# Performance work log

Hardware: AMD Instinct MI355X
Metric: run time of the kernel (lower is better)

## Reference

```python
import jax, jax.numpy as jnp
import numpy as np

N_NODES = 50000
N_EDGES = 1600000
D = 64          # n_atom_basis = n_filters
NB = 25         # n_basis (RBF)
L = 3           # n_interactions
CUTOFF = 5.0
MAX_Z = 100


def swish(x):
    return x * jax.nn.sigmoid(x)


def setup_inputs() -> dict:
    key = jax.random.key(0)
    ks = jax.random.split(key, 20)
    z = jax.random.randint(ks[0], (N_NODES,), 0, MAX_Z)
    src = jax.random.randint(ks[1], (N_EDGES,), 0, N_NODES)
    dst = jax.random.randint(ks[2], (N_EDGES,), 0, N_NODES)
    rij = jax.random.uniform(ks[3], (N_EDGES,), jnp.float32, 0.3, CUTOFF)
    s = 1.0 / np.sqrt(D)
    emb = jax.random.normal(ks[4], (MAX_Z, D), jnp.float32) * 0.1
    emb = emb.at[0].set(0.0)  # padding_idx=0
    Win = jax.random.normal(ks[5], (L, D, D), jnp.float32) * s
    Wf1 = jax.random.normal(ks[6], (L, NB, D), jnp.float32) * (1.0 / np.sqrt(NB))
    bf1 = jnp.zeros((L, D), jnp.float32)
    Wf2 = jax.random.normal(ks[7], (L, D, D), jnp.float32) * s
    bf2 = jnp.zeros((L, D), jnp.float32)
    Wo1 = jax.random.normal(ks[8], (L, D, D), jnp.float32) * s
    bo1 = jnp.zeros((L, D), jnp.float32)
    Wo2 = jax.random.normal(ks[9], (L, D, D), jnp.float32) * s
    bo2 = jnp.zeros((L, D), jnp.float32)
    gn_alpha = jnp.ones((L, D), jnp.float32)
    gn_gamma = jnp.ones((L, D), jnp.float32)
    gn_beta = jnp.zeros((L, D), jnp.float32)
    return dict(z=z, src=src, dst=dst, rij=rij, emb=emb, Win=Win,
                Wf1=Wf1, bf1=bf1, Wf2=Wf2, bf2=bf2,
                Wo1=Wo1, bo1=bo1, Wo2=Wo2, bo2=bo2,
                gn_alpha=gn_alpha, gn_gamma=gn_gamma, gn_beta=gn_beta)


def reference(z, src, dst, rij, emb, Win, Wf1, bf1, Wf2, bf2,
              Wo1, bo1, Wo2, bo2, gn_alpha, gn_gamma, gn_beta):
    n = z.shape[0]
    # GaussianSmearing(0, cutoff, n_basis)
    offsets = jnp.linspace(0.0, CUTOFF, NB)
    width = offsets[1] - offsets[0]
    coeff = -0.5 / (width * width)
    fij = jnp.exp(coeff * (rij[:, None] - offsets[None, :]) ** 2)  # [E, NB]
    # CosineCutoff
    C = 0.5 * (jnp.cos(rij * (np.pi / CUTOFF)) + 1.0) * (rij < CUTOFF)  # [E]

    feat = emb[z]  # [N, D]
    for l in range(L):
        # cfconv: in2f (no bias), filter MLP gated by cutoff, gather*W, scatter-sum
        x1 = feat @ Win[l]                                            # [N, D]
        W = swish(fij @ Wf1[l] + bf1[l]) @ Wf2[l] + bf2[l]            # [E, D]
        W = W * C[:, None]
        m = x1[src] * W                                               # [E, D]
        agg = jax.ops.segment_sum(m, dst, num_segments=n)             # [N, D]
        # f2out: Dense+swish, Dense; residual
        y = swish(agg @ Wo1[l] + bo1[l]) @ Wo2[l] + bo2[l]
        feat = feat + y
        # GraphNorm over all nodes (single graph)
        mean = feat.mean(axis=0)
        h = feat - gn_alpha[l] * mean
        var = (h * h).mean(axis=0)
        feat = gn_gamma[l] * h * jax.lax.rsqrt(var + 1e-5) + gn_beta[l]

    # softmax readout: per-feature attention over nodes
    w = jax.nn.softmax(feat, axis=0)
    pooled = (w * feat).sum(axis=0)  # [D]
    return feat, pooled
```

## Files before the change

### kernel.cpp

```cpp
#include <hip/hip_runtime.h>
#include <hip/hip_bf16.h>
#include <math.h>

#define D64 64
#define KTAB 4096
#define TROWS (KTAB + 1)

typedef unsigned int uint4a __attribute__((ext_vector_type(4), aligned(4)));
typedef __attribute__((ext_vector_type(8))) short bf16x8;
typedef __attribute__((ext_vector_type(4))) float f32x4;

__device__ __forceinline__ void atomAddF(float* p, float v) {
  __hip_atomic_fetch_add(p, v, __ATOMIC_RELAXED, __HIP_MEMORY_SCOPE_AGENT);
}
__device__ __forceinline__ float swishf(float x) { return x / (1.0f + expf(-x)); }
__device__ __forceinline__ float bx(unsigned short s) {
  return __uint_as_float((unsigned)s << 16);
}
__device__ __forceinline__ unsigned short f2b(float f) {
  unsigned u = __float_as_uint(f);
  return (unsigned short)((u + 0x7FFFu + ((u >> 16) & 1u)) >> 16);
}

__global__ void k_init(const int* __restrict__ z, const float* __restrict__ emb,
                       float* __restrict__ feat, int total) {
  int idx = blockIdx.x * 256 + threadIdx.x;
  if (idx < total) feat[idx] = emb[z[idx >> 6] * D64 + (idx & 63)];
}

__global__ void k_wprep(const float* __restrict__ Win, const float* __restrict__ Wo1,
                        const float* __restrict__ Wo2, unsigned short* __restrict__ Wb) {
  int idx = blockIdx.x * 256 + threadIdx.x;
  if (idx >= 3 * 3 * 64 * 8) return;
  const int fr = idx & 7;
  const int lane = (idx >> 3) & 63;
  const int m = (idx >> 9) % 3;
  const int l = idx / 1536;
  const int ct = fr >> 1, ks = fr & 1;
  const int c = ct * 16 + (lane & 15);
  const int k0 = ks * 32 + (lane >> 4) * 8;
  const float* W = (m == 0 ? Win : (m == 1 ? Wo1 : Wo2)) + (size_t)l * D64 * D64;
  unsigned short* o = &Wb[(size_t)((l * 3 + m) * 64 + lane) * 64 + fr * 8];
#pragma unroll
  for (int j = 0; j < 8; ++j) o[j] = f2b(W[(k0 + j) * D64 + c]);
}

__global__ __launch_bounds__(256) void k_hist64(const int* __restrict__ dst,
                                                int* __restrict__ bcnt, int E) {
  __shared__ int c[64];
  if (threadIdx.x < 64) c[threadIdx.x] = 0;
  __syncthreads();
  const int step = gridDim.x * blockDim.x * 4;
  for (int i = (blockIdx.x * blockDim.x + threadIdx.x) * 4; i < E; i += step) {
    if (i + 4 <= E) {
      int4 d = *(const int4*)&dst[i];
      atomicAdd(&c[d.x >> 10], 1);
      atomicAdd(&c[d.y >> 10], 1);
      atomicAdd(&c[d.z >> 10], 1);
      atomicAdd(&c[d.w >> 10], 1);
    } else {
      for (int q = i; q < E; ++q) atomicAdd(&c[dst[q] >> 10], 1);
    }
  }
  __syncthreads();
  if (threadIdx.x < 64 && c[threadIdx.x] > 0)
    atomicAdd(&bcnt[threadIdx.x], c[threadIdx.x]);
}

__global__ void k_scan64(const int* __restrict__ bcnt, int* __restrict__ bbase,
                         int* __restrict__ gcur) {
  const int t = threadIdx.x;
  int v = bcnt[t];
  int x = v;
  for (int o = 1; o < 64; o <<= 1) {
    int y = __shfl_up(x, o);
    if (t >= o) x += y;
  }
  bbase[t] = x - v;
  gcur[t] = x - v;
  if (t == 63) bbase[64] = x;
}

__global__ __launch_bounds__(256) void k_part(const int* __restrict__ src,
                                              const int* __restrict__ dst,
                                              const float* __restrict__ rij,
                                              int* __restrict__ gcur,
                                              uint2* __restrict__ rec, int E) {
  __shared__ uint2 ord[2048];
  __shared__ unsigned char obk[2048];
  __shared__ int cnt[64], cbase[64], cpos[64], gpos[64];
  __shared__ int tot_s;
  const int tid = threadIdx.x;
  for (int c = blockIdx.x; c * 2048 < E; c += gridDim.x) {
    const int s0 = c * 2048;
    if (tid < 64) cnt[tid] = 0;
    __syncthreads();
    const int i0 = s0 + tid * 8;
    int dd[8], ss[8];
    float rr[8];
    bool val[8];
    if (i0 + 8 <= E) {
      int4 d0 = *(const int4*)&dst[i0];
      int4 d1 = *(const int4*)&dst[i0 + 4];
      int4 sa = *(const int4*)&src[i0];
      int4 sb2 = *(const int4*)&src[i0 + 4];
      float4 r0 = *(const float4*)&rij[i0];
      float4 r1 = *(const float4*)&rij[i0 + 4];
      dd[0] = d0.x; dd[1] = d0.y; dd[2] = d0.z; dd[3] = d0.w;
      dd[4] = d1.x; dd[5] = d1.y; dd[6] = d1.z; dd[7] = d1.w;
      ss[0] = sa.x; ss[1] = sa.y; ss[2] = sa.z; ss[3] = sa.w;
      ss[4] = sb2.x; ss[5] = sb2.y; ss[6] = sb2.z; ss[7] = sb2.w;
      rr[0] = r0.x; rr[1] = r0.y; rr[2] = r0.z; rr[3] = r0.w;
      rr[4] = r1.x; rr[5] = r1.y; rr[6] = r1.z; rr[7] = r1.w;
#pragma unroll
      for (int q = 0; q < 8; ++q) val[q] = true;
    } else {
#pragma unroll
      for (int q = 0; q < 8; ++q) {
        int i = i0 + q;
        val[q] = (i < E);
        if (val[q]) { dd[q] = dst[i]; ss[q] = src[i]; rr[q] = rij[i]; }
        else { dd[q] = 0; ss[q] = 0; rr[q] = 0.0f; }
      }
    }
    int bk[8];
    unsigned ry[8];
#pragma unroll
    for (int q = 0; q < 8; ++q) {
      bk[q] = dd[q] >> 10;
      int k = (int)(rr[q] * ((float)KTAB * 0.2f) + 0.5f);
      if (k > KTAB) k = KTAB;
      ry[q] = ((unsigned)ss[q] << 16) | (unsigned)k;
      if (val[q]) atomicAdd(&cnt[bk[q]], 1);
    }
    __syncthreads();
    if (tid < 64) {
      int v = cnt[tid];
      int x = v;
      for (int o = 1; o < 64; o <<= 1) {
        int y = __shfl_up(x, o);
        if (tid >= o) x += y;
      }
      cbase[tid] = x - v;
      cpos[tid] = x - v;
      if (tid == 63) tot_s = x;
    }
    __syncthreads();
#pragma unroll
    for (int q = 0; q < 8; ++q) {
      if (val[q]) {
        int slot = atomicAdd(&cpos[bk[q]], 1);
        ord[slot] = make_uint2((unsigned)dd[q], ry[q]);
        obk[slot] = (unsigned char)bk[q];
      }
    }
    __syncthreads();
    if (tid < 64 && cnt[tid] > 0) gpos[tid] = atomicAdd(&gcur[tid], cnt[tid]);
    __syncthreads();
    const int tot = tot_s;
    for (int t = tid; t < tot; t += 256) {
      int b2 = obk[t];
      rec[gpos[b2] + (t - cbase[b2])] = ord[t];
    }
    __syncthreads();
  }
}

__global__ __launch_bounds__(1024) void k_build(const uint2* __restrict__ rec,
                                                const int* __restrict__ bbase,
                                                int* __restrict__ rp,
                                                unsigned* __restrict__ ep, int n) {
  __shared__ int cnt[1024];
  __shared__ int curl[1024];
  const int tid = threadIdx.x;
  const int b = blockIdx.x;
  const int lo = bbase[b], hi = bbase[b + 1];
  cnt[tid] = 0;
  __syncthreads();
  for (int i = lo + tid; i < hi; i += 1024)
    atomicAdd(&cnt[rec[i].x & 1023], 1);
  __syncthreads();
  const int v = cnt[tid];
  for (int o = 1; o < 1024; o <<= 1) {
    int t = (tid >= o) ? cnt[tid - o] : 0;
    __syncthreads();
    cnt[tid] += t;
    __syncthreads();
  }
  const int excl = cnt[tid] - v;
  curl[tid] = excl;
  const int node = (b << 10) + tid;
  if (node <= n) rp[node] = lo + excl;
  __syncthreads();
  for (int i = lo + tid; i < hi; i += 1024) {
    uint2 e = rec[i];
    int pos = lo + atomicAdd(&curl[e.x & 1023], 1);
    ep[pos] = e.y;
  }
}

__global__ __launch_bounds__(256) void k_tables(const float* __restrict__ Wf1,
                                                const float* __restrict__ bf1,
                                                const float* __restrict__ Wf2,
                                                const float* __restrict__ bf2,
                                                __hip_bfloat16* __restrict__ Tb) {
  __shared__ float w1[25 * D64];
  __shared__ float w2[D64 * D64];
  __shared__ float rb[4][D64];
  const int lane = threadIdx.x & 63;
  const int wsl = threadIdx.x >> 6;
  const int l = blockIdx.x / 129;
  const int gb = blockIdx.x % 129;
  for (int i = threadIdx.x; i < 25 * D64; i += 256) w1[i] = Wf1[l * 25 * D64 + i];
  for (int i = threadIdx.x; i < D64 * D64; i += 256) w2[i] = Wf2[l * D64 * D64 + i];
  __syncthreads();
  const float bias1 = bf1[l * D64 + lane];
  const float bias2 = bf2[l * D64 + lane];
  const float width = 5.0f / 24.0f;
  const float coeff = -0.5f / (width * width);
  for (int gi = 0; gi < 8; ++gi) {
    const int g = gb * 32 + wsl * 8 + gi;
    if (g >= TROWS) break;
    const float r = (float)g * (5.0f / KTAB);
    float fv = 0.0f;
    if (lane < 25) { float ddv = r - (float)lane * width; fv = expf(coeff * ddv * ddv); }
    rb[wsl][lane] = fv;
    float a1 = bias1;
#pragma unroll
    for (int b = 0; b < 25; ++b)
      a1 = fmaf(rb[wsl][b], w1[b * D64 + lane], a1);
    float sw = swishf(a1);
    rb[wsl][lane] = sw;
    float a2 = bias2;
#pragma unroll
    for (int k = 0; k < D64; ++k)
      a2 = fmaf(rb[wsl][k], w2[k * D64 + lane], a2);
    float C = (r < 5.0f) ? 0.5f * (cosf(r * 0.62831853f) + 1.0f) : 0.0f;
    Tb[(size_t)(l * TROWS + g) * D64 + lane] = __float2bfloat16(a2 * C);
  }
}

__global__ void k_nid(float* __restrict__ stats) {
  int d = threadIdx.x;
  stats[128 + d] = 1.0f;
  stats[192 + d] = 0.0f;
}

__global__ __launch_bounds__(256) void k_x1(const float* __restrict__ feat,
                                            const unsigned short* __restrict__ Wb,
                                            const float* __restrict__ stats,
                                            __hip_bfloat16* __restrict__ x1, int n) {
  const int lane = threadIdx.x & 63;
  const int r16 = lane & 15;
  const int kg = lane >> 4;
  unsigned short* __restrict__ x1u = (unsigned short*)x1;
  const unsigned short* wl = Wb + (size_t)lane * 64;
  bf16x8 bw[4][2];
#pragma unroll
  for (int ct = 0; ct < 4; ++ct)
#pragma unroll
    for (int ks = 0; ks < 2; ++ks)
      bw[ct][ks] = *(const bf16x8*)&wl[(ct * 2 + ks) * 8];
  float sca[2][8], sha[2][8];
#pragma unroll
  for (int ks = 0; ks < 2; ++ks) {
    const int k0 = ks * 32 + kg * 8;
#pragma unroll
    for (int j = 0; j < 8; ++j) {
      sca[ks][j] = stats[128 + k0 + j];
      sha[ks][j] = stats[192 + k0 + j];
    }
  }
  const int ntile = (n + 15) >> 4;
  const int wid = (blockIdx.x * blockDim.x + threadIdx.x) >> 6;
  const int nw = (gridDim.x * blockDim.x) >> 6;
  for (int t = wid; t < ntile; t += nw) {
    const int base = t * 16;
    int ra = base + r16; if (ra > n - 1) ra = n - 1;
    bf16x8 a[2];
#pragma unroll
    for (int ks = 0; ks < 2; ++ks) {
      const float* p = &feat[(size_t)ra * D64 + ks * 32 + kg * 8];
      bf16x8 v;
#pragma unroll
      for (int j = 0; j < 8; ++j) v[j] = (short)f2b(fmaf(p[j], sca[ks][j], sha[ks][j]));
      a[ks] = v;
    }
    f32x4 acc[4];
#pragma unroll
    for (int ct = 0; ct < 4; ++ct) {
      f32x4 z = {0.0f, 0.0f, 0.0f, 0.0f};
      z = __builtin_amdgcn_mfma_f32_16x16x32_bf16(a[0], bw[ct][0], z, 0, 0, 0);
      z = __builtin_amdgcn_mfma_f32_16x16x32_bf16(a[1], bw[ct][1], z, 0, 0, 0);
      acc[ct] = z;
    }
#pragma unroll
    for (int ct = 0; ct < 4; ++ct)
#pragma unroll
      for (int r = 0; r < 4; ++r) {
        const int rm = base + kg * 4 + r;
        if (rm < n) x1u[(size_t)rm * D64 + ct * 16 + r16] = f2b(acc[ct][r]);
      }
  }
}

__global__ __launch_bounds__(256) void k_gather(const __hip_bfloat16* __restrict__ x1,
                                                const __hip_bfloat16* __restrict__ Tb,
                                                const unsigned* __restrict__ ep,
                                                const int* __restrict__ rp,
                                                unsigned short* __restrict__ aggb, int n) {
  const int lane = threadIdx.x & 63;
  const int half = lane >> 5;
  const int fl = lane & 31;
  const unsigned short* __restrict__ x1u = (const unsigned short*)x1;
  const unsigned short* __restrict__ Tu = (const unsigned short*)Tb;
  const int wid = (blockIdx.x * blockDim.x + threadIdx.x) >> 6;
  const int nw = (gridDim.x * blockDim.x) >> 6;
  for (int nd = wid; nd < n; nd += nw) {
    const int j0 = rp[nd], j1 = rp[nd + 1];
    float ax0 = 0.0f, ay0 = 0.0f, ax1 = 0.0f, ay1 = 0.0f;
    int j = j0;
    for (; j + 8 <= j1; j += 8) {
      const uint4a uu = *(const uint4a*)(ep + j + 4 * half);
      const unsigned u0 = uu.x, u1 = uu.y, u2 = uu.z, u3 = uu.w;
      const ushort2 xA = *(const ushort2*)&x1u[(size_t)(u0 >> 16) * D64 + fl * 2];
      const ushort2 xB = *(const ushort2*)&x1u[(size_t)(u1 >> 16) * D64 + fl * 2];
      const ushort2 xC = *(const ushort2*)&x1u[(size_t)(u2 >> 16) * D64 + fl * 2];
      const ushort2 xD = *(const ushort2*)&x1u[(size_t)(u3 >> 16) * D64 + fl * 2];
      const ushort2 tA = *(const ushort2*)&Tu[(size_t)(u0 & 0x1FFFu) * D64 + fl * 2];
      const ushort2 tB = *(const ushort2*)&Tu[(size_t)(u1 & 0x1FFFu) * D64 + fl * 2];
      const ushort2 tC = *(const ushort2*)&Tu[(size_t)(u2 & 0x1FFFu) * D64 + fl * 2];
      const ushort2 tD = *(const ushort2*)&Tu[(size_t)(u3 & 0x1FFFu) * D64 + fl * 2];
      ax0 = fmaf(bx(xA.x), bx(tA.x), ax0);
      ay0 = fmaf(bx(xA.y), bx(tA.y), ay0);
      ax1 = fmaf(bx(xB.x), bx(tB.x), ax1);
      ay1 = fmaf(bx(xB.y), bx(tB.y), ay1);
      ax0 = fmaf(bx(xC.x), bx(tC.x), ax0);
      ay0 = fmaf(bx(xC.y), bx(tC.y), ay0);
      ax1 = fmaf(bx(xD.x), bx(tD.x), ax1);
      ay1 = fmaf(bx(xD.y), bx(tD.y), ay1);
    }
    for (; j + 2 <= j1; j += 2) {
      const unsigned u = ep[j + half];
      const ushort2 xr = *(const ushort2*)&x1u[(size_t)(u >> 16) * D64 + fl * 2];
      const ushort2 tw = *(const ushort2*)&Tu[(size_t)(u & 0x1FFFu) * D64 + fl * 2];
      ax0 = fmaf(bx(xr.x), bx(tw.x), ax0);
      ay0 = fmaf(bx(xr.y), bx(tw.y), ay0);
    }
    if (j < j1 && half == 0) {
      const unsigned u = ep[j];
      const ushort2 xr = *(const ushort2*)&x1u[(size_t)(u >> 16) * D64 + fl * 2];
      const ushort2 tw = *(const ushort2*)&Tu[(size_t)(u & 0x1FFFu) * D64 + fl * 2];
      ax0 = fmaf(bx(xr.x), bx(tw.x), ax0);
      ay0 = fmaf(bx(xr.y), bx(tw.y), ay0);
    }
    float ax = ax0 + ax1, ay = ay0 + ay1;
    ax += __shfl_xor(ax, 32);
    ay += __shfl_xor(ay, 32);
    if (half == 0) {
      unsigned pk = ((unsigned)f2b(ay) << 16) | (unsigned)f2b(ax);
      *(unsigned*)&aggb[(size_t)nd * D64 + fl * 2] = pk;
    }
  }
}

__global__ __launch_bounds__(256) void k_out(const unsigned short* __restrict__ aggb,
                                             const unsigned short* __restrict__ Wb1,
                                             const unsigned short* __restrict__ Wb2,
                                             const float* __restrict__ bo1,
                                             const float* __restrict__ bo2,
                                             const float* __restrict__ nstats,
                                             float* __restrict__ feat,
                                             float* __restrict__ part, int n) {
  __shared__ __align__(16) unsigned short tl[4][16 * 72];
  __shared__ float redp[4][128];
  const int lane = threadIdx.x & 63;
  const int wsl = threadIdx.x >> 6;
  const int r16 = lane & 15;
  const int kg = lane >> 4;
  const unsigned short* wl1 = Wb1 + (size_t)lane * 64;
  const unsigned short* wl2 = Wb2 + (size_t)lane * 64;
  bf16x8 bw1[4][2], bw2[4][2];
#pragma unroll
  for (int ct = 0; ct < 4; ++ct)
#pragma unroll
    for (int ks = 0; ks < 2; ++ks) {
      bw1[ct][ks] = *(const bf16x8*)&wl1[(ct * 2 + ks) * 8];
      bw2[ct][ks] = *(const bf16x8*)&wl2[(ct * 2 + ks) * 8];
    }
  float b1c[4], b2c[4], scc[4], shc[4];
#pragma unroll
  for (int ct = 0; ct < 4; ++ct) {
    b1c[ct] = bo1[ct * 16 + r16];
    b2c[ct] = bo2[ct * 16 + r16];
    scc[ct] = nstats[128 + ct * 16 + r16];
    shc[ct] = nstats[192 + ct * 16 + r16];
  }
  float sf[4] = {0, 0, 0, 0}, sf2[4] = {0, 0, 0, 0};
  unsigned short* tw = tl[wsl];
  const int ntile = (n + 15) >> 4;
  const int wid = (blockIdx.x * blockDim.x + threadIdx.x) >> 6;
  const int nw = (gridDim.x * blockDim.x) >> 6;
  for (int t = wid; t < ntile; t += nw) {
    const int base = t * 16;
    int ra = base + r16; if (ra > n - 1) ra = n - 1;
    bf16x8 a1[2];
#pragma unroll
    for (int ks = 0; ks < 2; ++ks)
      a1[ks] = *(const bf16x8*)&aggb[(size_t)ra * D64 + ks * 32 + kg * 8];
    f32x4 acc[4];
#pragma unroll
    for (int ct = 0; ct < 4; ++ct) {
      f32x4 z = {0.0f, 0.0f, 0.0f, 0.0f};
      z = __builtin_amdgcn_mfma_f32_16x16x32_bf16(a1[0], bw1[ct][0], z, 0, 0, 0);
      z = __builtin_amdgcn_mfma_f32_16x16x32_bf16(a1[1], bw1[ct][1], z, 0, 0, 0);
      acc[ct] = z;
    }
#pragma unroll
    for (int ct = 0; ct < 4; ++ct)
#pragma unroll
      for (int r = 0; r < 4; ++r)
        tw[(kg * 4 + r) * 72 + ct * 16 + r16] = f2b(swishf(acc[ct][r] + b1c[ct]));
    bf16x8 a2[2];
#pragma unroll
    for (int ks = 0; ks < 2; ++ks)
      a2[ks] = *(const bf16x8*)&tw[r16 * 72 + ks * 32 + kg * 8];
    f32x4 acc2[4];
#pragma unroll
    for (int ct = 0; ct < 4; ++ct) {
      f32x4 z = {0.0f, 0.0f, 0.0f, 0.0f};
      z = __builtin_amdgcn_mfma_f32_16x16x32_bf16(a2[0], bw2[ct][0], z, 0, 0, 0);
      z = __builtin_amdgcn_mfma_f32_16x16x32_bf16(a2[1], bw2[ct][1], z, 0, 0, 0);
      acc2[ct] = z;
    }
#pragma unroll
    for (int ct = 0; ct < 4; ++ct)
#pragma unroll
      for (int r = 0; r < 4; ++r) {
        const int rm = base + kg * 4 + r;
        if (rm < n) {
          const size_t ix = (size_t)rm * D64 + ct * 16 + r16;
          float fv = fmaf(feat[ix], scc[ct], shc[ct]);
          float fn = fv + acc2[ct][r] + b2c[ct];
          feat[ix] = fn;
          sf[ct] += fn;
          sf2[ct] += fn * fn;
        }
      }
  }
#pragma unroll
  for (int ct = 0; ct < 4; ++ct) {
    sf[ct] += __shfl_xor(sf[ct], 16);
    sf[ct] += __shfl_xor(sf[ct], 32);
    sf2[ct] += __shfl_xor(sf2[ct], 16);
    sf2[ct] += __shfl_xor(sf2[ct], 32);
  }
  if (kg == 0) {
#pragma unroll
    for (int ct = 0; ct < 4; ++ct) {
      redp[wsl][ct * 16 + r16] = sf[ct];
      redp[wsl][64 + ct * 16 + r16] = sf2[ct];
    }
  }
  __syncthreads();
  if (threadIdx.x < 128) {
    float v = redp[0][threadIdx.x] + redp[1][threadIdx.x] +
              redp[2][threadIdx.x] + redp[3][threadIdx.x];
    atomAddF(&part[(blockIdx.x & 63) * 128 + threadIdx.x], v);
  }
}

__global__ void k_nfin(float* __restrict__ part, float* __restrict__ stats,
                       const float* __restrict__ al, const float* __restrict__ ga,
                       const float* __restrict__ be, int n) {
  const int t = threadIdx.x;
  float s = 0.0f;
#pragma unroll 8
  for (int b = 0; b < 64; ++b) s += part[b * 128 + t];
  __shared__ float red[128];
  red[t] = s;
#pragma unroll 8
  for (int b = 0; b < 64; ++b) part[b * 128 + t] = 0.0f;
  __syncthreads();
  if (t < 64) {
    float invN = 1.0f / (float)n;
    float mu = red[t] * invN;
    float ex2 = red[64 + t] * invN;
    float a = al[t];
    float var = ex2 - (2.0f * a - a * a) * mu * mu;
    float sc = ga[t] * rsqrtf(var + 1e-5f);
    stats[128 + t] = sc;
    stats[192 + t] = be[t] - sc * a * mu;
  }
}

__global__ __launch_bounds__(256) void k_pool(float* __restrict__ feat,
                                              const float* __restrict__ stats,
                                              float* __restrict__ part, int n) {
  __shared__ float redp[4][128];
  const int lane = threadIdx.x & 63;
  const int wsl = threadIdx.x >> 6;
  const float sc = stats[128 + lane], sh = stats[192 + lane];
  float s1 = 0.0f, s2 = 0.0f;
  const int wid = (blockIdx.x * blockDim.x + threadIdx.x) >> 6;
  const int nw = (gridDim.x * blockDim.x) >> 6;
  int base = wid * 4;
  const int stride = nw * 4;
  for (; base + 4 <= n; base += stride) {
    float f0 = feat[(size_t)(base + 0) * D64 + lane];
    float f1 = feat[(size_t)(base + 1) * D64 + lane];
    float f2 = feat[(size_t)(base + 2) * D64 + lane];
    float f3 = feat[(size_t)(base + 3) * D64 + lane];
    f0 = fmaf(f0, sc, sh);
    f1 = fmaf(f1, sc, sh);
    f2 = fmaf(f2, sc, sh);
    f3 = fmaf(f3, sc, sh);
    feat[(size_t)(base + 0) * D64 + lane] = f0;
    feat[(size_t)(base + 1) * D64 + lane] = f1;
    feat[(size_t)(base + 2) * D64 + lane] = f2;
    feat[(size_t)(base + 3) * D64 + lane] = f3;
    float e0 = expf(f0 - 20.0f);
    float e1 = expf(f1 - 20.0f);
    float e2 = expf(f2 - 20.0f);
    float e3 = expf(f3 - 20.0f);
    s1 += (e0 + e1) + (e2 + e3);
    s2 += fmaf(f0, e0, f1 * e1) + fmaf(f2, e2, f3 * e3);
  }
  for (int r = base; r < n; ++r) {
    float f = fmaf(feat[(size_t)r * D64 + lane], sc, sh);
    feat[(size_t)r * D64 + lane] = f;
    float e = expf(f - 20.0f);
    s1 += e;
    s2 += f * e;
  }
  redp[wsl][lane] = s1;
  redp[wsl][64 + lane] = s2;
  __syncthreads();
  if (threadIdx.x < 128) {
    float v = redp[0][threadIdx.x] + redp[1][threadIdx.x] +
              redp[2][threadIdx.x] + redp[3][threadIdx.x];
    atomAddF(&part[(blockIdx.x & 63) * 128 + threadIdx.x], v);
  }
}

__global__ void k_pooled(const float* __restrict__ part, float* __restrict__ out) {
  int d = threadIdx.x;
  float s1 = 0.0f, s2 = 0.0f;
#pragma unroll 8
  for (int b = 0; b < 64; ++b) {
    s1 += part[b * 128 + d];
    s2 += part[b * 128 + 64 + d];
  }
  out[d] = s2 / s1;
}

extern "C" void kernel_launch(void* const* d_in, const int* in_sizes, int n_in,
                              void* d_out, int out_size, void* d_ws, size_t ws_size,
                              hipStream_t stream) {
  const int* z = (const int*)d_in[0];
  const int* src = (const int*)d_in[1];
  const int* dst = (const int*)d_in[2];
  const float* rij = (const float*)d_in[3];
  const float* emb = (const float*)d_in[4];
  const float* Win = (const float*)d_in[5];
  const float* Wf1 = (const float*)d_in[6];
  const float* bf1 = (const float*)d_in[7];
  const float* Wf2 = (const float*)d_in[8];
  const float* bf2 = (const float*)d_in[9];
  const float* Wo1 = (const float*)d_in[10];
  const float* bo1 = (const float*)d_in[11];
  const float* Wo2 = (const float*)d_in[12];
  const float* bo2 = (const float*)d_in[13];
  const float* gal = (const float*)d_in[14];
  const float* gga = (const float*)d_in[15];
  const float* gbe = (const float*)d_in[16];
  const int n = in_sizes[0];
  const int E = in_sizes[1];
  (void)n_in; (void)out_size; (void)ws_size;

  float* feat = (float*)d_out;
  float* pooled = feat + (size_t)n * D64;

  char* w = (char*)d_ws;
  size_t off = 0;
  auto take = [&](size_t bytes) {
    size_t o = (off + 255) & ~(size_t)255;
    off = o + bytes;
    return (void*)(w + o);
  };
  __hip_bfloat16* x1 = (__hip_bfloat16*)take((size_t)n * D64 * 2);
  size_t aggrec = ((size_t)n * D64 * 2 > (size_t)E * 8) ? (size_t)n * D64 * 2
                                                        : (size_t)E * 8;
  unsigned short* aggb = (unsigned short*)take(aggrec);
  uint2* rec = (uint2*)aggb;
  float* stats = (float*)take(256 * 4);
  float* part = (float*)take(64 * 128 * 4);
  __hip_bfloat16* Tb = (__hip_bfloat16*)take((size_t)3 * TROWS * D64 * 2);
  unsigned short* Wb = (unsigned short*)take((size_t)9 * 64 * 64 * 2);
  int* rp = (int*)take((size_t)(n + 1) * 4);
  unsigned* ep = (unsigned*)take((size_t)E * 4);
  int* bbase = (int*)take(65 * 4);
  int* gcur = (int*)take(64 * 4);
  int* bcnt = (int*)take(64 * 4);

  hipMemsetAsync(bcnt, 0, 64 * 4, stream);
  hipMemsetAsync(part, 0, 64 * 128 * 4, stream);
  k_init<<<(n * D64 + 255) / 256, 256, 0, stream>>>(z, emb, feat, n * D64);
  k_wprep<<<18, 256, 0, stream>>>(Win, Wo1, Wo2, Wb);
  k_hist64<<<256, 256, 0, stream>>>(dst, bcnt, E);
  k_scan64<<<1, 64, 0, stream>>>(bcnt, bbase, gcur);
  k_part<<<784, 256, 0, stream>>>(src, dst, rij, gcur, rec, E);
  k_build<<<64, 1024, 0, stream>>>(rec, bbase, rp, ep, n);
  k_tables<<<3 * 129, 256, 0, stream>>>(Wf1, bf1, Wf2, bf2, Tb);
  k_nid<<<1, 64, 0, stream>>>(stats);

  for (int l = 0; l < 3; ++l) {
    k_x1<<<784, 256, 0, stream>>>(feat, Wb + (size_t)(l * 3 + 0) * 64 * 64,
                                  stats, x1, n);
    k_gather<<<2048, 256, 0, stream>>>(x1, Tb + (size_t)l * TROWS * D64,
                                       ep, rp, aggb, n);
    k_out<<<784, 256, 0, stream>>>(aggb,
                                   Wb + (size_t)(l * 3 + 1) * 64 * 64,
                                   Wb + (size_t)(l * 3 + 2) * 64 * 64,
                                   bo1 + l * D64, bo2 + l * D64, stats,
                                   feat, part, n);
    k_nfin<<<1, 128, 0, stream>>>(part, stats, gal + l * D64, gga + l * D64, gbe + l * D64, n);
  }

  k_pool<<<1024, 256, 0, stream>>>(feat, stats, part, n);
  k_pooled<<<1, 64, 0, stream>>>(part, pooled);
}
```

Measured before the change: 352.2 us.

## Merge setup kernels, fold GraphNorm finalize into output kernel, unroll gather

Several small setup kernels are merged into fewer launches: init, weight prep and histogram go into one kernel, and partitioning and filter-table building into another, with blocks dispatched by block index. The per-layer GraphNorm finalize kernel is removed. The last-arriving block of the output kernel now computes the statistics using an atomic ticket counter. The gather loop gains a 16-edge unrolled path to keep more loads in flight. This cuts launch count and serial gaps at the cost of a grid-wide ticket synchronisation and higher register pressure in the gather.

```diff
diff --git a/kernel.cpp b/kernel.cpp
--- a/kernel.cpp
+++ b/kernel.cpp
@@ -5,6 +5,8 @@
 #define D64 64
 #define KTAB 4096
 #define TROWS (KTAB + 1)
+#define PARTB 784
+#define TABB 387
 
 typedef unsigned int uint4a __attribute__((ext_vector_type(4), aligned(4)));
 typedef __attribute__((ext_vector_type(8))) short bf16x8;
@@ -13,6 +15,9 @@
 __device__ __forceinline__ void atomAddF(float* p, float v) {
   __hip_atomic_fetch_add(p, v, __ATOMIC_RELAXED, __HIP_MEMORY_SCOPE_AGENT);
 }
+__device__ __forceinline__ float atomLoadF(const float* p) {
+  return __hip_atomic_load(p, __ATOMIC_RELAXED, __HIP_MEMORY_SCOPE_AGENT);
+}
 __device__ __forceinline__ float swishf(float x) { return x / (1.0f + expf(-x)); }
 __device__ __forceinline__ float bx(unsigned short s) {
   return __uint_as_float((unsigned)s << 16);
@@ -22,53 +27,60 @@
   return (unsigned short)((u + 0x7FFFu + ((u >> 16) & 1u)) >> 16);
 }
 
-__global__ void k_init(const int* __restrict__ z, const float* __restrict__ emb,
-                       float* __restrict__ feat, int total) {
-  int idx = blockIdx.x * 256 + threadIdx.x;
-  if (idx < total) feat[idx] = emb[z[idx >> 6] * D64 + (idx & 63)];
-}
-
-__global__ void k_wprep(const float* __restrict__ Win, const float* __restrict__ Wo1,
-                        const float* __restrict__ Wo2, unsigned short* __restrict__ Wb) {
-  int idx = blockIdx.x * 256 + threadIdx.x;
-  if (idx >= 3 * 3 * 64 * 8) return;
-  const int fr = idx & 7;
-  const int lane = (idx >> 3) & 63;
-  const int m = (idx >> 9) % 3;
-  const int l = idx / 1536;
-  const int ct = fr >> 1, ks = fr & 1;
-  const int c = ct * 16 + (lane & 15);
-  const int k0 = ks * 32 + (lane >> 4) * 8;
-  const float* W = (m == 0 ? Win : (m == 1 ? Wo1 : Wo2)) + (size_t)l * D64 * D64;
-  unsigned short* o = &Wb[(size_t)((l * 3 + m) * 64 + lane) * 64 + fr * 8];
-#pragma unroll
-  for (int j = 0; j < 8; ++j) o[j] = f2b(W[(k0 + j) * D64 + c]);
-}
-
-__global__ __launch_bounds__(256) void k_hist64(const int* __restrict__ dst,
-                                                int* __restrict__ bcnt, int E) {
+__global__ __launch_bounds__(256) void k_pre(const int* __restrict__ z,
+                                             const float* __restrict__ emb,
+                                             float* __restrict__ feat,
+                                             const float* __restrict__ Win,
+                                             const float* __restrict__ Wo1,
+                                             const float* __restrict__ Wo2,
+                                             unsigned short* __restrict__ Wb,
+                                             const int* __restrict__ dst,
+                                             int* __restrict__ bcnt,
+                                             int total, int nbInit, int E) {
   __shared__ int c[64];
-  if (threadIdx.x < 64) c[threadIdx.x] = 0;
-  __syncthreads();
-  const int step = gridDim.x * blockDim.x * 4;
-  for (int i = (blockIdx.x * blockDim.x + threadIdx.x) * 4; i < E; i += step) {
-    if (i + 4 <= E) {
-      int4 d = *(const int4*)&dst[i];
-      atomicAdd(&c[d.x >> 10], 1);
-      atomicAdd(&c[d.y >> 10], 1);
-      atomicAdd(&c[d.z >> 10], 1);
-      atomicAdd(&c[d.w >> 10], 1);
-    } else {
-      for (int q = i; q < E; ++q) atomicAdd(&c[dst[q] >> 10], 1);
-    }
-  }
-  __syncthreads();
-  if (threadIdx.x < 64 && c[threadIdx.x] > 0)
-    atomicAdd(&bcnt[threadIdx.x], c[threadIdx.x]);
+  const int bid = blockIdx.x;
+  if (bid < nbInit) {
+    int idx = bid * 256 + threadIdx.x;
+    if (idx < total) feat[idx] = emb[z[idx >> 6] * D64 + (idx & 63)];
+  } else if (bid < nbInit + 18) {
+    int idx = (bid - nbInit) * 256 + threadIdx.x;
+    if (idx < 3 * 3 * 64 * 8) {
+      const int fr = idx & 7;
+      const int lane = (idx >> 3) & 63;
+      const int m = (idx >> 9) % 3;
+      const int l = idx / 1536;
+      const int ct = fr >> 1, ks = fr & 1;
+      const int cc = ct * 16 + (lane & 15);
+      const int k0 = ks * 32 + (lane >> 4) * 8;
+      const float* W = (m == 0 ? Win : (m == 1 ? Wo1 : Wo2)) + (size_t)l * D64 * D64;
+      unsigned short* o = &Wb[(size_t)((l * 3 + m) * 64 + lane) * 64 + fr * 8];
+#pragma unroll
+      for (int j = 0; j < 8; ++j) o[j] = f2b(W[(k0 + j) * D64 + cc]);
+    }
+  } else {
+    const int hb = bid - nbInit - 18;
+    if (threadIdx.x < 64) c[threadIdx.x] = 0;
+    __syncthreads();
+    const int step = 256 * 256 * 4;
+    for (int i = (hb * 256 + threadIdx.x) * 4; i < E; i += step) {
+      if (i + 4 <= E) {
+        int4 d = *(const int4*)&dst[i];
+        atomicAdd(&c[d.x >> 10], 1);
+        atomicAdd(&c[d.y >> 10], 1);
+        atomicAdd(&c[d.z >> 10], 1);
+        atomicAdd(&c[d.w >> 10], 1);
+      } else {
+        for (int q = i; q < E; ++q) atomicAdd(&c[dst[q] >> 10], 1);
+      }
+    }
+    __syncthreads();
+    if (threadIdx.x < 64 && c[threadIdx.x] > 0)
+      atomicAdd(&bcnt[threadIdx.x], c[threadIdx.x]);
+  }
 }
 
 __global__ void k_scan64(const int* __restrict__ bcnt, int* __restrict__ bbase,
-                         int* __restrict__ gcur) {
+                         int* __restrict__ gcur, float* __restrict__ stats) {
   const int t = threadIdx.x;
   int v = bcnt[t];
   int x = v;
@@ -79,90 +91,143 @@
   bbase[t] = x - v;
   gcur[t] = x - v;
   if (t == 63) bbase[64] = x;
-}
-
-__global__ __launch_bounds__(256) void k_part(const int* __restrict__ src,
+  stats[128 + t] = 1.0f;
+  stats[192 + t] = 0.0f;
+}
+
+struct PartS {
+  uint2 ord[2048];
+  int cnt[64], cbase[64], cpos[64], gpos[64];
+  int tot;
+  unsigned char obk[2048];
+};
+struct TabS {
+  float w1[25 * D64];
+  float w2[D64 * D64];
+  float rb[4][D64];
+};
+
+__global__ __launch_bounds__(256) void k_ptab(const int* __restrict__ src,
                                               const int* __restrict__ dst,
                                               const float* __restrict__ rij,
                                               int* __restrict__ gcur,
-                                              uint2* __restrict__ rec, int E) {
-  __shared__ uint2 ord[2048];
-  __shared__ unsigned char obk[2048];
-  __shared__ int cnt[64], cbase[64], cpos[64], gpos[64];
-  __shared__ int tot_s;
+                                              uint2* __restrict__ rec, int E,
+                                              const float* __restrict__ Wf1,
+                                              const float* __restrict__ bf1,
+                                              const float* __restrict__ Wf2,
+                                              const float* __restrict__ bf2,
+                                              __hip_bfloat16* __restrict__ Tb) {
+  __shared__ __align__(16) char smem[sizeof(TabS)];
   const int tid = threadIdx.x;
-  for (int c = blockIdx.x; c * 2048 < E; c += gridDim.x) {
-    const int s0 = c * 2048;
-    if (tid < 64) cnt[tid] = 0;
+  if (blockIdx.x < PARTB) {
+    PartS& S = *(PartS*)smem;
+    for (int c = blockIdx.x; c * 2048 < E; c += PARTB) {
+      const int s0 = c * 2048;
+      if (tid < 64) S.cnt[tid] = 0;
+      __syncthreads();
+      const int i0 = s0 + tid * 8;
+      int dd[8], ss[8];
+      float rr[8];
+      bool val[8];
+      if (i0 + 8 <= E) {
+        int4 d0 = *(const int4*)&dst[i0];
+        int4 d1 = *(const int4*)&dst[i0 + 4];
+        int4 sa = *(const int4*)&src[i0];
+        int4 sb2 = *(const int4*)&src[i0 + 4];
+        float4 r0 = *(const float4*)&rij[i0];
+        float4 r1 = *(const float4*)&rij[i0 + 4];
+        dd[0] = d0.x; dd[1] = d0.y; dd[2] = d0.z; dd[3] = d0.w;
+        dd[4] = d1.x; dd[5] = d1.y; dd[6] = d1.z; dd[7] = d1.w;
+        ss[0] = sa.x; ss[1] = sa.y; ss[2] = sa.z; ss[3] = sa.w;
+        ss[4] = sb2.x; ss[5] = sb2.y; ss[6] = sb2.z; ss[7] = sb2.w;
+        rr[0] = r0.x; rr[1] = r0.y; rr[2] = r0.z; rr[3] = r0.w;
+        rr[4] = r1.x; rr[5] = r1.y; rr[6] = r1.z; rr[7] = r1.w;
+#pragma unroll
+        for (int q = 0; q < 8; ++q) val[q] = true;
+      } else {
+#pragma unroll
+        for (int q = 0; q < 8; ++q) {
+          int i = i0 + q;
+          val[q] = (i < E);
+          if (val[q]) { dd[q] = dst[i]; ss[q] = src[i]; rr[q] = rij[i]; }
+          else { dd[q] = 0; ss[q] = 0; rr[q] = 0.0f; }
+        }
+      }
+      int bk[8];
+      unsigned ry[8];
+#pragma unroll
+      for (int q = 0; q < 8; ++q) {
+        bk[q] = dd[q] >> 10;
+        int k = (int)(rr[q] * ((float)KTAB * 0.2f) + 0.5f);
+        if (k > KTAB) k = KTAB;
+        ry[q] = ((unsigned)ss[q] << 16) | (unsigned)k;
+        if (val[q]) atomicAdd(&S.cnt[bk[q]], 1);
+      }
+      __syncthreads();
+      if (tid < 64) {
+        int v = S.cnt[tid];
+        int x = v;
+        for (int o = 1; o < 64; o <<= 1) {
+          int y = __shfl_up(x, o);
+          if (tid >= o) x += y;
+        }
+        S.cbase[tid] = x - v;
+        S.cpos[tid] = x - v;
+        if (tid == 63) S.tot = x;
+      }
+      __syncthreads();
+#pragma unroll
+      for (int q = 0; q < 8; ++q) {
+        if (val[q]) {
+          int slot = atomicAdd(&S.cpos[bk[q]], 1);
+          S.ord[slot] = make_uint2((unsigned)dd[q], ry[q]);
+          S.obk[slot] = (unsigned char)bk[q];
+        }
+      }
+      __syncthreads();
+      if (tid < 64 && S.cnt[tid] > 0) S.gpos[tid] = atomicAdd(&gcur[tid], S.cnt[tid]);
+      __syncthreads();
+      const int tot = S.tot;
+      for (int t = tid; t < tot; t += 256) {
+        int b2 = S.obk[t];
+        rec[S.gpos[b2] + (t - S.cbase[b2])] = S.ord[t];
+      }
+      __syncthreads();
+    }
+  } else {
+    TabS& T = *(TabS*)smem;
+    const int tb = blockIdx.x - PARTB;
+    const int lane = tid & 63;
+    const int wsl = tid >> 6;
+    const int l = tb / 129;
+    const int gb = tb % 129;
+    for (int i = tid; i < 25 * D64; i += 256) T.w1[i] = Wf1[l * 25 * D64 + i];
+    for (int i = tid; i < D64 * D64; i += 256) T.w2[i] = Wf2[l * D64 * D64 + i];
     __syncthreads();
-    const int i0 = s0 + tid * 8;
-    int dd[8], ss[8];
-    float rr[8];
-    bool val[8];
-    if (i0 + 8 <= E) {
-      int4 d0 = *(const int4*)&dst[i0];
-      int4 d1 = *(const int4*)&dst[i0 + 4];
-      int4 sa = *(const int4*)&src[i0];
-      int4 sb2 = *(const int4*)&src[i0 + 4];
-      float4 r0 = *(const float4*)&rij[i0];
-      float4 r1 = *(const float4*)&rij[i0 + 4];
-      dd[0] = d0.x; dd[1] = d0.y; dd[2] = d0.z; dd[3] = d0.w;
-      dd[4] = d1.x; dd[5] = d1.y; dd[6] = d1.z; dd[7] = d1.w;
-      ss[0] = sa.x; ss[1] = sa.y; ss[2] = sa.z; ss[3] = sa.w;
-      ss[4] = sb2.x; ss[5] = sb2.y; ss[6] = sb2.z; ss[7] = sb2.w;
-      rr[0] = r0.x; rr[1] = r0.y; rr[2] = r0.z; rr[3] = r0.w;
-      rr[4] = r1.x; rr[5] = r1.y; rr[6] = r1.z; rr[7] = r1.w;
-#pragma unroll
-      for (int q = 0; q < 8; ++q) val[q] = true;
-    } else {
-#pragma unroll
-      for (int q = 0; q < 8; ++q) {
-        int i = i0 + q;
-        val[q] = (i < E);
-        if (val[q]) { dd[q] = dst[i]; ss[q] = src[i]; rr[q] = rij[i]; }
-        else { dd[q] = 0; ss[q] = 0; rr[q] = 0.0f; }
-      }
-    }
-    int bk[8];
-    unsigned ry[8];
-#pragma unroll
-    for (int q = 0; q < 8; ++q) {
-      bk[q] = dd[q] >> 10;
-      int k = (int)(rr[q] * ((float)KTAB * 0.2f) + 0.5f);
-      if (k > KTAB) k = KTAB;
-      ry[q] = ((unsigned)ss[q] << 16) | (unsigned)k;
-      if (val[q]) atomicAdd(&cnt[bk[q]], 1);
-    }
-    __syncthreads();
-    if (tid < 64) {
-      int v = cnt[tid];
-      int x = v;
-      for (int o = 1; o < 64; o <<= 1) {
-        int y = __shfl_up(x, o);
-        if (tid >= o) x += y;
-      }
-      cbase[tid] = x - v;
-      cpos[tid] = x - v;
-      if (tid == 63) tot_s = x;
-    }
-    __syncthreads();
-#pragma unroll
-    for (int q = 0; q < 8; ++q) {
-      if (val[q]) {
-        int slot = atomicAdd(&cpos[bk[q]], 1);
-        ord[slot] = make_uint2((unsigned)dd[q], ry[q]);
-        obk[slot] = (unsigned char)bk[q];
-      }
-    }
-    __syncthreads();
-    if (tid < 64 && cnt[tid] > 0) gpos[tid] = atomicAdd(&gcur[tid], cnt[tid]);
-    __syncthreads();
-    const int tot = tot_s;
-    for (int t = tid; t < tot; t += 256) {
-      int b2 = obk[t];
-      rec[gpos[b2] + (t - cbase[b2])] = ord[t];
-    }
-    __syncthreads();
+    const float bias1 = bf1[l * D64 + lane];
+    const float bias2 = bf2[l * D64 + lane];
+    const float width = 5.0f / 24.0f;
+    const float coeff = -0.5f / (width * width);
+    for (int gi = 0; gi < 8; ++gi) {
+      const int g = gb * 32 + wsl * 8 + gi;
+      if (g >= TROWS) break;
+      const float r = (float)g * (5.0f / KTAB);
+      float fv = 0.0f;
+      if (lane < 25) { float ddv = r - (float)lane * width; fv = expf(coeff * ddv * ddv); }
+      T.rb[wsl][lane] = fv;
+      float a1 = bias1;
+#pragma unroll
+      for (int b = 0; b < 25; ++b)
+        a1 = fmaf(T.rb[wsl][b], T.w1[b * D64 + lane], a1);
+      float sw = swishf(a1);
+      T.rb[wsl][lane] = sw;
+      float a2 = bias2;
+#pragma unroll
+      for (int k = 0; k < D64; ++k)
+        a2 = fmaf(T.rb[wsl][k], T.w2[k * D64 + lane], a2);
+      float C = (r < 5.0f) ? 0.5f * (cosf(r * 0.62831853f) + 1.0f) : 0.0f;
+      Tb[(size_t)(l * TROWS + g) * D64 + lane] = __float2bfloat16(a2 * C);
+    }
   }
 }
 
@@ -197,53 +262,6 @@
     int pos = lo + atomicAdd(&curl[e.x & 1023], 1);
     ep[pos] = e.y;
   }
-}
-
-__global__ __launch_bounds__(256) void k_tables(const float* __restrict__ Wf1,
-                                                const float* __restrict__ bf1,
-                                                const float* __restrict__ Wf2,
-                                                const float* __restrict__ bf2,
-                                                __hip_bfloat16* __restrict__ Tb) {
-  __shared__ float w1[25 * D64];
-  __shared__ float w2[D64 * D64];
-  __shared__ float rb[4][D64];
-  const int lane = threadIdx.x & 63;
-  const int wsl = threadIdx.x >> 6;
-  const int l = blockIdx.x / 129;
-  const int gb = blockIdx.x % 129;
-  for (int i = threadIdx.x; i < 25 * D64; i += 256) w1[i] = Wf1[l * 25 * D64 + i];
-  for (int i = threadIdx.x; i < D64 * D64; i += 256) w2[i] = Wf2[l * D64 * D64 + i];
-  __syncthreads();
-  const float bias1 = bf1[l * D64 + lane];
-  const float bias2 = bf2[l * D64 + lane];
-  const float width = 5.0f / 24.0f;
-  const float coeff = -0.5f / (width * width);
-  for (int gi = 0; gi < 8; ++gi) {
-    const int g = gb * 32 + wsl * 8 + gi;
-    if (g >= TROWS) break;
-    const float r = (float)g * (5.0f / KTAB);
-    float fv = 0.0f;
-    if (lane < 25) { float ddv = r - (float)lane * width; fv = expf(coeff * ddv * ddv); }
-    rb[wsl][lane] = fv;
-    float a1 = bias1;
-#pragma unroll
-    for (int b = 0; b < 25; ++b)
-      a1 = fmaf(rb[wsl][b], w1[b * D64 + lane], a1);
-    float sw = swishf(a1);
-    rb[wsl][lane] = sw;
-    float a2 = bias2;
-#pragma unroll
-    for (int k = 0; k < D64; ++k)
-      a2 = fmaf(rb[wsl][k], w2[k * D64 + lane], a2);
-    float C = (r < 5.0f) ? 0.5f * (cosf(r * 0.62831853f) + 1.0f) : 0.0f;
-    Tb[(size_t)(l * TROWS + g) * D64 + lane] = __float2bfloat16(a2 * C);
-  }
-}
-
-__global__ void k_nid(float* __restrict__ stats) {
-  int d = threadIdx.x;
-  stats[128 + d] = 1.0f;
-  stats[192 + d] = 0.0f;
 }
 
 __global__ __launch_bounds__(256) void k_x1(const float* __restrict__ feat,
@@ -320,6 +338,28 @@
     const int j0 = rp[nd], j1 = rp[nd + 1];
     float ax0 = 0.0f, ay0 = 0.0f, ax1 = 0.0f, ay1 = 0.0f;
     int j = j0;
+    for (; j + 16 <= j1; j += 16) {
+      const uint4a ua = *(const uint4a*)(ep + j + 8 * half);
+      const uint4a ub = *(const uint4a*)(ep + j + 8 * half + 4);
+      const unsigned u[8] = {ua.x, ua.y, ua.z, ua.w, ub.x, ub.y, ub.z, ub.w};
+      ushort2 xv[8], tv[8];
+#pragma unroll
+      for (int q = 0; q < 8; ++q)
+        xv[q] = *(const ushort2*)&x1u[(size_t)(u[q] >> 16) * D64 + fl * 2];
+#pragma unroll
+      for (int q = 0; q < 8; ++q)
+        tv[q] = *(const ushort2*)&Tu[(size_t)(u[q] & 0x1FFFu) * D64 + fl * 2];
+#pragma unroll
+      for (int q = 0; q < 8; ++q) {
+        if (q & 1) {
+          ax1 = fmaf(bx(xv[q].x), bx(tv[q].x), ax1);
+          ay1 = fmaf(bx(xv[q].y), bx(tv[q].y), ay1);
+        } else {
+          ax0 = fmaf(bx(xv[q].x), bx(tv[q].x), ax0);
+          ay0 = fmaf(bx(xv[q].y), bx(tv[q].y), ay0);
+        }
+      }
+    }
     for (; j + 8 <= j1; j += 8) {
       const uint4a uu = *(const uint4a*)(ep + j + 4 * half);
       const unsigned u0 = uu.x, u1 = uu.y, u2 = uu.z, u3 = uu.w;
@@ -364,16 +404,22 @@
   }
 }
 
-__global__ __launch_bounds__(256) void k_out(const unsigned short* __restrict__ aggb,
-                                             const unsigned short* __restrict__ Wb1,
-                                             const unsigned short* __restrict__ Wb2,
-                                             const float* __restrict__ bo1,
-                                             const float* __restrict__ bo2,
-                                             const float* __restrict__ nstats,
-                                             float* __restrict__ feat,
-                                             float* __restrict__ part, int n) {
+__global__ __launch_bounds__(256) void k_outn(const unsigned short* __restrict__ aggb,
+                                              const unsigned short* __restrict__ Wb1,
+                                              const unsigned short* __restrict__ Wb2,
+                                              const float* __restrict__ bo1,
+                                              const float* __restrict__ bo2,
+                                              float* __restrict__ stats,
+                                              float* __restrict__ feat,
+                                              float* __restrict__ part,
+                                              int* __restrict__ ticket,
+                                              const float* __restrict__ al,
+                                              const float* __restrict__ ga,
+                                              const float* __restrict__ be, int n) {
   __shared__ __align__(16) unsigned short tl[4][16 * 72];
   __shared__ float redp[4][128];
+  __shared__ float red[128];
+  __shared__ int lastflag;
   const int lane = threadIdx.x & 63;
   const int wsl = threadIdx.x >> 6;
   const int r16 = lane & 15;
@@ -393,8 +439,8 @@
   for (int ct = 0; ct < 4; ++ct) {
     b1c[ct] = bo1[ct * 16 + r16];
     b2c[ct] = bo2[ct * 16 + r16];
-    scc[ct] = nstats[128 + ct * 16 + r16];
-    shc[ct] = nstats[192 + ct * 16 + r16];
+    scc[ct] = stats[128 + ct * 16 + r16];
+    shc[ct] = stats[192 + ct * 16 + r16];
   }
   float sf[4] = {0, 0, 0, 0}, sf2[4] = {0, 0, 0, 0};
   unsigned short* tw = tl[wsl];
@@ -468,19 +514,23 @@
               redp[2][threadIdx.x] + redp[3][threadIdx.x];
     atomAddF(&part[(blockIdx.x & 63) * 128 + threadIdx.x], v);
   }
-}
-
-__global__ void k_nfin(float* __restrict__ part, float* __restrict__ stats,
-                       const float* __restrict__ al, const float* __restrict__ ga,
-                       const float* __restrict__ be, int n) {
+  __syncthreads();
+  if (threadIdx.x == 0) {
+    __threadfence();
+    int t = __hip_atomic_fetch_add(ticket, 1, __ATOMIC_ACQ_REL, __HIP_MEMORY_SCOPE_AGENT);
+    lastflag = (t == (int)gridDim.x - 1);
+  }
+  __syncthreads();
+  if (!lastflag) return;
   const int t = threadIdx.x;
-  float s = 0.0f;
+  if (t < 128) {
+    float s = 0.0f;
 #pragma unroll 8
-  for (int b = 0; b < 64; ++b) s += part[b * 128 + t];
-  __shared__ float red[128];
-  red[t] = s;
+    for (int b = 0; b < 64; ++b) s += atomLoadF(&part[b * 128 + t]);
+    red[t] = s;
 #pragma unroll 8
-  for (int b = 0; b < 64; ++b) part[b * 128 + t] = 0.0f;
+    for (int b = 0; b < 64; ++b) part[b * 128 + t] = 0.0f;
+  }
   __syncthreads();
   if (t < 64) {
     float invN = 1.0f / (float)n;
@@ -492,6 +542,7 @@
     stats[128 + t] = sc;
     stats[192 + t] = be[t] - sc * a * mu;
   }
+  if (t == 0) *ticket = 0;
 }
 
 __global__ __launch_bounds__(256) void k_pool(float* __restrict__ feat,
@@ -601,30 +652,33 @@
   unsigned* ep = (unsigned*)take((size_t)E * 4);
   int* bbase = (int*)take(65 * 4);
   int* gcur = (int*)take(64 * 4);
-  int* bcnt = (int*)take(64 * 4);
-
-  hipMemsetAsync(bcnt, 0, 64 * 4, stream);
+  int* misc = (int*)take(128 * 4);
+  int* bcnt = misc;
+  int* ticket = misc + 64;
+
+  const int total = n * D64;
+  const int nbInit = (total + 255) / 256;
+
+  hipMemsetAsync(misc, 0, 128 * 4, stream);
   hipMemsetAsync(part, 0, 64 * 128 * 4, stream);
-  k_init<<<(n * D64 + 255) / 256, 256, 0, stream>>>(z, emb, feat, n * D64);
-  k_wprep<<<18, 256, 0, stream>>>(Win, Wo1, Wo2, Wb);
-  k_hist64<<<256, 256, 0, stream>>>(dst, bcnt, E);
-  k_scan64<<<1, 64, 0, stream>>>(bcnt, bbase, gcur);
-  k_part<<<784, 256, 0, stream>>>(src, dst, rij, gcur, rec, E);
+  k_pre<<<nbInit + 18 + 256, 256, 0, stream>>>(z, emb, feat, Win, Wo1, Wo2, Wb,
+                                               dst, bcnt, total, nbInit, E);
+  k_scan64<<<1, 64, 0, stream>>>(bcnt, bbase, gcur, stats);
+  k_ptab<<<PARTB + TABB, 256, 0, stream>>>(src, dst, rij, gcur, rec, E,
+                                           Wf1, bf1, Wf2, bf2, Tb);
   k_build<<<64, 1024, 0, stream>>>(rec, bbase, rp, ep, n);
-  k_tables<<<3 * 129, 256, 0, stream>>>(Wf1, bf1, Wf2, bf2, Tb);
-  k_nid<<<1, 64, 0, stream>>>(stats);
 
   for (int l = 0; l < 3; ++l) {
     k_x1<<<784, 256, 0, stream>>>(feat, Wb + (size_t)(l * 3 + 0) * 64 * 64,
                                   stats, x1, n);
     k_gather<<<2048, 256, 0, stream>>>(x1, Tb + (size_t)l * TROWS * D64,
                                        ep, rp, aggb, n);
-    k_out<<<784, 256, 0, stream>>>(aggb,
-                                   Wb + (size_t)(l * 3 + 1) * 64 * 64,
-                                   Wb + (size_t)(l * 3 + 2) * 64 * 64,
-                                   bo1 + l * D64, bo2 + l * D64, stats,
-                                   feat, part, n);
-    k_nfin<<<1, 128, 0, stream>>>(part, stats, gal + l * D64, gga + l * D64, gbe + l * D64, n);
+    k_outn<<<784, 256, 0, stream>>>(aggb,
+                                    Wb + (size_t)(l * 3 + 1) * 64 * 64,
+                                    Wb + (size_t)(l * 3 + 2) * 64 * 64,
+                                    bo1 + l * D64, bo2 + l * D64, stats,
+                                    feat, part, ticket,
+                                    gal + l * D64, gga + l * D64, gbe + l * D64, n);
   }
 
   k_pool<<<1024, 256, 0, stream>>>(feat, stats, part, n);
```

New measurement: 452.0 us. 28.3% more time.
